# Optimization experiments

Hardware: AMD Instinct MI355X
Metric: run time of the kernel (lower is better)

## Reference

```python
import jax, jax.numpy as jnp
import numpy as np

CS = 5           # context_size
PAD = CS // 2    # spatial padding
EPS = 1e-12      # torch F.normalize eps


def setup_inputs() -> dict:
    key = jax.random.key(0)
    k1, k2, k3 = jax.random.split(key, 3)
    B, C, H, W = 8, 1024, 64, 64
    OC, INC = 1024, C + CS * CS  # 1049 input channels to 1x1 conv
    feature = jax.random.normal(k1, (B, C, H, W), dtype=jnp.float32)
    conv_w = jax.random.normal(k2, (OC, INC), dtype=jnp.float32) * 0.02
    conv_b = jax.random.normal(k3, (OC,), dtype=jnp.float32) * 0.02
    return {"feature": feature, "conv_w": conv_w, "conv_b": conv_b}


def reference(feature, conv_w, conv_b):
    b, c, h, w = feature.shape
    # L2-normalize over channel dim (torch normalize: x / max(||x||, eps))
    norm = jnp.sqrt(jnp.sum(feature * feature, axis=1, keepdims=True))
    fn = feature / jnp.maximum(norm, EPS)
    fp = jnp.pad(fn, ((0, 0), (0, 0), (PAD, PAD), (PAD, PAD)))
    # Windowed cosine-similarity cost volume: 25 fixed shifts (small static loop)
    sims = []
    for cc in range(CS):      # column shift (outer, matches torch ordering)
        for r in range(CS):   # row shift
            sims.append(jnp.sum(fp[:, :, r:h + r, cc:w + cc] * fn, axis=1))
    vol = jnp.stack(sims, axis=1)              # [b, 25, h, w]
    x = jnp.concatenate([feature, vol], axis=1)  # [b, c+25, h, w]
    # 1x1 conv == per-pixel GEMM over channels
    out = jnp.einsum('bihw,oi->bohw', x, conv_w) + conv_b[None, :, None, None]
    return jax.nn.relu(out)
```

## Files before the change

### kernel.cpp

```cpp
#include <hip/hip_runtime.h>
#include <stdint.h>

#define C_DIM 1024
#define HW    4096
#define KPAD  1056
#define KIN   1049
#define NPIX  32768

typedef __bf16 bf16x8 __attribute__((ext_vector_type(8)));
typedef float  f32x4  __attribute__((ext_vector_type(4)));
typedef unsigned short u16x8 __attribute__((ext_vector_type(8)));

typedef const __attribute__((address_space(1))) void* gas_t;
typedef __attribute__((address_space(3))) void* las_t;

__device__ __forceinline__ unsigned short f2bf(float f) {
  unsigned u = __float_as_uint(f);
  unsigned r = u + 0x7FFFu + ((u >> 16) & 1u);
  return (unsigned short)(r >> 16);
}

__global__ __launch_bounds__(256) void prep_w(const float* __restrict__ cw,
                                              unsigned short* __restrict__ wb) {
  int o = blockIdx.x;
  for (int k = threadIdx.x; k < KPAD; k += 256) {
    float v = (k < KIN) ? cw[(size_t)o * KIN + k] : 0.0f;
    wb[(size_t)o * KPAD + k] = f2bf(v);
  }
}

__global__ __launch_bounds__(256) void pack_norm(const float* __restrict__ feat,
                                                 unsigned short* __restrict__ xb,
                                                 float* __restrict__ inv_norm,
                                                 int p_base) {
  __shared__ float tile[64][65];
  __shared__ float red[4][64];
  int t   = threadIdx.x;
  int p0l = blockIdx.x * 64;
  int p0g = p_base + p0l;
  int b   = p0g >> 12;
  int hw0 = p0g & 4095;
  int pl = t & 63;
  int q  = t >> 6;
  const float* fb = feat + (size_t)b * C_DIM * HW + hw0;
  float sumsq = 0.0f;
  for (int cc = 0; cc < 16; ++cc) {
#pragma unroll
    for (int i = 0; i < 16; ++i) {
      int cl = q + 4 * i;
      float v = fb[(size_t)(cc * 64 + cl) * HW + pl];
      sumsq += v * v;
      tile[cl][pl] = v;
    }
    __syncthreads();
#pragma unroll
    for (int r = 0; r < 2; ++r) {
      int id = t + r * 256;
      int pr = id >> 3;
      int c8 = id & 7;
      u16x8 hv;
#pragma unroll
      for (int e = 0; e < 8; ++e) hv[e] = f2bf(tile[c8 * 8 + e][pr]);
      size_t row = (size_t)(p0l + pr) * KPAD + cc * 64 + c8 * 8;
      *reinterpret_cast<u16x8*>(xb + row) = hv;
    }
    __syncthreads();
  }
  red[q][pl] = sumsq;
  __syncthreads();
  if (t < 64) {
    float s = red[0][t] + red[1][t] + red[2][t] + red[3][t];
    inv_norm[p0g + t] = 1.0f / fmaxf(sqrtf(s), 1e-12f);
  }
}

__global__ __launch_bounds__(256) void corr_part(const float* __restrict__ feat,
                                                 float* __restrict__ part,
                                                 int b_base, int npix_s) {
  __shared__ float tile[4][8][72];
  int t = threadIdx.x;
  int bid = blockIdx.x;
  int chunk = bid & 3;
  int ht = (bid >> 2) & 15;
  int bl = bid >> 6;
  int b  = b_base + bl;
  int h0 = ht * 4;
  int r0 = t >> 6;
  int w  = t & 63;
  {
    int ch = t >> 6, r = (t >> 3) & 7, c = t & 7;
    int col = (c < 2) ? c : (64 + c);
    tile[ch][r][col] = 0.0f;
  }
  __syncthreads();
  const float* fb = feat + (size_t)b * C_DIM * HW;
  int c0 = chunk * 256;
  int h_lo = h0 - 2 + r0;
  int h_hi = h0 + 2 + r0;
  bool v_lo = (h_lo >= 0);
  bool v_hi = (h_hi < 64);
  size_t off_lo = (size_t)(v_lo ? h_lo : 0) * 64 + w;
  size_t off_hi = (size_t)(v_hi ? h_hi : 0) * 64 + w;
  float acc[25];
#pragma unroll
  for (int j = 0; j < 25; ++j) acc[j] = 0.0f;
  for (int ci0 = 0; ci0 < 256; ci0 += 4) {
    float lo[4], hi[4];
#pragma unroll
    for (int cc = 0; cc < 4; ++cc) {
      size_t cb = (size_t)(c0 + ci0 + cc) * HW;
      lo[cc] = v_lo ? fb[cb + off_lo] : 0.0f;
      hi[cc] = v_hi ? fb[cb + off_hi] : 0.0f;
    }
    __syncthreads();
#pragma unroll
    for (int cc = 0; cc < 4; ++cc) {
      tile[cc][r0][2 + w]     = lo[cc];
      tile[cc][r0 + 4][2 + w] = hi[cc];
    }
    __syncthreads();
#pragma unroll
    for (int cc = 0; cc < 4; ++cc) {
      float rv[5][5];
#pragma unroll
      for (int dr5 = 0; dr5 < 5; ++dr5) {
        const float* rp = &tile[cc][r0 + dr5][w];
#pragma unroll
        for (int dc5 = 0; dc5 < 5; ++dc5) rv[dr5][dc5] = rp[dc5];
      }
      float center = rv[2][2];
#pragma unroll
      for (int dc5 = 0; dc5 < 5; ++dc5)
#pragma unroll
        for (int dr5 = 0; dr5 < 5; ++dr5)
          acc[dc5 * 5 + dr5] += rv[dr5][dc5] * center;
    }
  }
  int pl = bl * 4096 + (h0 + r0) * 64 + w;
#pragma unroll
  for (int j = 0; j < 25; ++j)
    part[(size_t)(chunk * 25 + j) * npix_s + pl] = acc[j];
}

__global__ __launch_bounds__(256) void corr_reduce(const float* __restrict__ part,
                                                   const float* __restrict__ inv_norm,
                                                   unsigned short* __restrict__ xb,
                                                   int p_base, int npix_s) {
  int pl = blockIdx.x * 256 + threadIdx.x;
  int pg = p_base + pl;
  int w = pg & 63, h = (pg >> 6) & 63, b = pg >> 12;
  float inv_c = inv_norm[pg];
  float vals[32];
#pragma unroll
  for (int j = 0; j < 32; ++j) {
    float v = 0.0f;
    if (j < 25) {
      int dc = j / 5 - 2, dr = j % 5 - 2;
      int hh = h + dr, ww = w + dc;
      if (hh >= 0 && hh < 64 && ww >= 0 && ww < 64) {
        float s = part[(size_t)(0 * 25 + j) * npix_s + pl]
                + part[(size_t)(1 * 25 + j) * npix_s + pl]
                + part[(size_t)(2 * 25 + j) * npix_s + pl]
                + part[(size_t)(3 * 25 + j) * npix_s + pl];
        v = s * inv_c * inv_norm[(b << 12) + (hh << 6) + ww];
      }
    }
    vals[j] = v;
  }
  unsigned short* xp = xb + (size_t)pl * KPAD + 1024;
#pragma unroll
  for (int g = 0; g < 4; ++g) {
    u16x8 pk;
#pragma unroll
    for (int e = 0; e < 8; ++e) pk[e] = f2bf(vals[g * 8 + e]);
    *reinterpret_cast<u16x8*>(xp + g * 8) = pk;
  }
}

__device__ __forceinline__ void stage_tile(const unsigned short* __restrict__ g,
                                           unsigned short* s, int t) {
#pragma unroll
  for (int r = 0; r < 2; ++r) {
    int idx = t + r * 256;
    int row = idx >> 2;
    int q = (idx & 3) ^ ((row >> 1) & 3);
    const unsigned short* gp = g + (size_t)row * KPAD + q * 8;
    unsigned short* sp = s + (t >> 6) * 512 + r * 2048;
    __builtin_amdgcn_global_load_lds((gas_t)gp, (las_t)sp, 16, 0, 0);
  }
}

__global__ __launch_bounds__(256, 2) void gemm_kernel(
    const unsigned short* __restrict__ xb, const unsigned short* __restrict__ wb,
    const float* __restrict__ bias, float* __restrict__ out,
    int p_base, int np) {
  __shared__ __align__(16) unsigned short sA[4096];
  __shared__ __align__(16) unsigned short sB[4096];
  int t = threadIdx.x;
  int lane = t & 63;
  int wid = t >> 6;
  int wm = wid >> 1, wn = wid & 1;
  int l15 = lane & 15, l4 = lane >> 4;
  int bid = blockIdx.x;
  int xcd = bid & 7;
  int j = bid >> 3;
  int o0 = (j & 7) * 128;
  int panel = xcd * (np >> 3) + (j >> 3);
  int p0l = panel * 128;

  f32x4 acc[4][4];
#pragma unroll
  for (int m = 0; m < 4; ++m)
#pragma unroll
    for (int n = 0; n < 4; ++n)
#pragma unroll
      for (int i = 0; i < 4; ++i) acc[m][n][i] = 0.0f;

  const unsigned short* A = wb + (size_t)o0 * KPAD;
  const unsigned short* B = xb + (size_t)p0l * KPAD;

  for (int kt = 0; kt < KPAD / 32; ++kt) {
    int k0 = kt * 32;
    stage_tile(A + k0, sA, t);
    stage_tile(B + k0, sB, t);
    __syncthreads();

    bf16x8 bf[4];
#pragma unroll
    for (int n = 0; n < 4; ++n) {
      int rr = wn * 64 + n * 16 + l15;
      int off = rr * 32 + ((l4 ^ ((rr >> 1) & 3)) * 8);
      bf[n] = *reinterpret_cast<const bf16x8*>(&sB[off]);
    }
#pragma unroll
    for (int m = 0; m < 4; ++m) {
      int ra = wm * 64 + m * 16 + l15;
      int off = ra * 32 + ((l4 ^ ((ra >> 1) & 3)) * 8);
      bf16x8 af = *reinterpret_cast<const bf16x8*>(&sA[off]);
#pragma unroll
      for (int n = 0; n < 4; ++n)
        acc[m][n] = __builtin_amdgcn_mfma_f32_16x16x32_bf16(af, bf[n], acc[m][n], 0, 0, 0);
    }
    __syncthreads();
  }

#pragma unroll
  for (int m = 0; m < 4; ++m) {
    int ob = o0 + wm * 64 + m * 16 + l4 * 4;
    float b0 = bias[ob], b1 = bias[ob + 1], b2 = bias[ob + 2], b3 = bias[ob + 3];
#pragma unroll
    for (int n = 0; n < 4; ++n) {
      int pg = p_base + p0l + wn * 64 + n * 16 + l15;
      int bb = pg >> 12, hw = pg & 4095;
      float* op = out + ((size_t)bb << 22) + hw;
      op[(size_t)(ob + 0) << 12] = fmaxf(acc[m][n][0] + b0, 0.0f);
      op[(size_t)(ob + 1) << 12] = fmaxf(acc[m][n][1] + b1, 0.0f);
      op[(size_t)(ob + 2) << 12] = fmaxf(acc[m][n][2] + b2, 0.0f);
      op[(size_t)(ob + 3) << 12] = fmaxf(acc[m][n][3] + b3, 0.0f);
    }
  }
}

extern "C" void kernel_launch(void* const* d_in, const int* in_sizes, int n_in,
                              void* d_out, int out_size, void* d_ws, size_t ws_size,
                              hipStream_t stream) {
  const float* feat = (const float*)d_in[0];
  const float* cw   = (const float*)d_in[1];
  const float* cb   = (const float*)d_in[2];
  float* out = (float*)d_out;

  const int NB = 8;
  const int npix_s = NB * 4096;

  char* ws = (char*)d_ws;
  size_t SZ_XS = (size_t)npix_s * KPAD * 2;
  size_t SZ_W  = (size_t)1024 * KPAD * 2;
  unsigned short* xb = (unsigned short*)(ws);
  unsigned short* wb = (unsigned short*)(ws + SZ_XS);
  float* inv_norm    = (float*)(ws + SZ_XS + SZ_W);
  float* part        = (float*)(ws + SZ_XS + SZ_W + (size_t)NPIX * 4);

  prep_w<<<1024, 256, 0, stream>>>(cw, wb);
  pack_norm<<<NB * 64, 256, 0, stream>>>(feat, xb, inv_norm, 0);
  corr_part<<<NB * 64, 256, 0, stream>>>(feat, part, 0, npix_s);
  corr_reduce<<<npix_s / 256, 256, 0, stream>>>(part, inv_norm, xb, 0, npix_s);
  gemm_kernel<<<8 * NB * 32, 256, 0, stream>>>(xb, wb, cb, out, 0, NB * 32);
}
```

Baseline: 451.8 us.

## Retile correlation kernel into 16-row strips with 4-pixel register blocking

The correlation partial kernel is restructured. Each block now covers a 16-row strip for one of 16 channel chunks instead of 4 rows for one of 4 chunks. Each thread computes 4 adjacent pixels from vectorized LDS window reads, and tiles are filled with direct global-to-LDS loads. The aim is to cut redundant halo loads and LDS reads per output and to drop the per-iteration register staging. The cost is a partial-sum buffer four times larger, which the reduce kernel must now write and sum over 16 chunks instead of 4.

```diff
diff --git a/kernel.cpp b/kernel.cpp
--- a/kernel.cpp
+++ b/kernel.cpp
@@ -6,9 +6,11 @@
 #define KPAD  1056
 #define KIN   1049
 #define NPIX  32768
+#define NCHUNK 16
 
 typedef __bf16 bf16x8 __attribute__((ext_vector_type(8)));
 typedef float  f32x4  __attribute__((ext_vector_type(4)));
+typedef float  f32x2  __attribute__((ext_vector_type(2)));
 typedef unsigned short u16x8 __attribute__((ext_vector_type(8)));
 
 typedef const __attribute__((address_space(1))) void* gas_t;
@@ -75,81 +77,77 @@
 }
 
 __global__ __launch_bounds__(256) void corr_part(const float* __restrict__ feat,
-                                                 float* __restrict__ part,
-                                                 int b_base, int npix_s) {
-  __shared__ float tile[4][8][72];
+                                                 float* __restrict__ part) {
+  __shared__ float lds4[4 + 1280 + 4];
+  float* tile = lds4 + 4;
   int t = threadIdx.x;
   int bid = blockIdx.x;
-  int chunk = bid & 3;
-  int ht = (bid >> 2) & 15;
-  int bl = bid >> 6;
-  int b  = b_base + bl;
-  int h0 = ht * 4;
-  int r0 = t >> 6;
-  int w  = t & 63;
-  {
-    int ch = t >> 6, r = (t >> 3) & 7, c = t & 7;
-    int col = (c < 2) ? c : (64 + c);
-    tile[ch][r][col] = 0.0f;
-  }
-  __syncthreads();
+  int chunk = bid & 15;
+  int strip = (bid >> 4) & 3;
+  int b     = bid >> 6;
+  int h0 = strip * 16;
+  int hr = t >> 4;
+  int w0 = (t & 15) * 4;
+  int wid = t >> 6;
+  int lane = t & 63;
+
   const float* fb = feat + (size_t)b * C_DIM * HW;
-  int c0 = chunk * 256;
-  int h_lo = h0 - 2 + r0;
-  int h_hi = h0 + 2 + r0;
-  bool v_lo = (h_lo >= 0);
-  bool v_hi = (h_hi < 64);
-  size_t off_lo = (size_t)(v_lo ? h_lo : 0) * 64 + w;
-  size_t off_hi = (size_t)(v_hi ? h_hi : 0) * 64 + w;
-  float acc[25];
-#pragma unroll
-  for (int j = 0; j < 25; ++j) acc[j] = 0.0f;
-  for (int ci0 = 0; ci0 < 256; ci0 += 4) {
-    float lo[4], hi[4];
-#pragma unroll
-    for (int cc = 0; cc < 4; ++cc) {
-      size_t cb = (size_t)(c0 + ci0 + cc) * HW;
-      lo[cc] = v_lo ? fb[cb + off_lo] : 0.0f;
-      hi[cc] = v_hi ? fb[cb + off_hi] : 0.0f;
-    }
-    __syncthreads();
-#pragma unroll
-    for (int cc = 0; cc < 4; ++cc) {
-      tile[cc][r0][2 + w]     = lo[cc];
-      tile[cc][r0 + 4][2 + w] = hi[cc];
-    }
-    __syncthreads();
-#pragma unroll
-    for (int cc = 0; cc < 4; ++cc) {
-      float rv[5][5];
-#pragma unroll
-      for (int dr5 = 0; dr5 < 5; ++dr5) {
-        const float* rp = &tile[cc][r0 + dr5][w];
-#pragma unroll
-        for (int dc5 = 0; dc5 < 5; ++dc5) rv[dr5][dc5] = rp[dc5];
-      }
-      float center = rv[2][2];
-#pragma unroll
-      for (int dc5 = 0; dc5 < 5; ++dc5)
-#pragma unroll
-        for (int dr5 = 0; dr5 < 5; ++dr5)
-          acc[dc5 * 5 + dr5] += rv[dr5][dc5] * center;
-    }
-  }
-  int pl = bl * 4096 + (h0 + r0) * 64 + w;
-#pragma unroll
-  for (int j = 0; j < 25; ++j)
-    part[(size_t)(chunk * 25 + j) * npix_s + pl] = acc[j];
+  int rA = t >> 4;
+  int cA = (t & 15) * 4;
+  int hA = min(max(h0 - 2 + rA, 0), 63);
+  int rB = 16 + wid;
+  int cB = lane;
+  int hB = min(max(h0 - 2 + rB, 0), 63);
+  const float* srcA = fb + hA * 64 + cA;
+  const float* srcB = fb + hB * 64 + cB;
+  float* dstA = tile + wid * 256;
+  float* dstB = tile + 1024 + wid * 64;
+
+  float acc[4][25];
+#pragma unroll
+  for (int j = 0; j < 4; ++j)
+#pragma unroll
+    for (int k = 0; k < 25; ++k) acc[j][k] = 0.0f;
+
+  int c0 = chunk * 64;
+  for (int ci = 0; ci < 64; ++ci) {
+    size_t coff = (size_t)(c0 + ci) * HW;
+    __builtin_amdgcn_global_load_lds((gas_t)(srcA + coff), (las_t)dstA, 16, 0, 0);
+    __builtin_amdgcn_global_load_lds((gas_t)(srcB + coff), (las_t)dstB, 4, 0, 0);
+    __syncthreads();
+
+    const float* rp2 = tile + (hr + 2) * 64 + w0;
+    f32x4 ctr4 = *reinterpret_cast<const f32x4*>(rp2);
+#pragma unroll
+    for (int r5 = 0; r5 < 5; ++r5) {
+      const float* rp = tile + (hr + r5) * 64 + w0;
+      f32x2 eL = *reinterpret_cast<const f32x2*>(rp - 2);
+      f32x4 cc4 = *reinterpret_cast<const f32x4*>(rp);
+      f32x2 eR = *reinterpret_cast<const f32x2*>(rp + 4);
+      float win[8] = {eL[0], eL[1], cc4[0], cc4[1], cc4[2], cc4[3], eR[0], eR[1]};
+#pragma unroll
+      for (int j = 0; j < 4; ++j)
+#pragma unroll
+        for (int dcv = 0; dcv < 5; ++dcv)
+          acc[j][dcv * 5 + r5] += win[j + dcv] * ctr4[j];
+    }
+    __syncthreads();
+  }
+
+  int p0 = b * 4096 + (h0 + hr) * 64 + w0;
+#pragma unroll
+  for (int jj = 0; jj < 25; ++jj) {
+    f32x4 v = {acc[0][jj], acc[1][jj], acc[2][jj], acc[3][jj]};
+    *reinterpret_cast<f32x4*>(&part[(size_t)(chunk * 25 + jj) * NPIX + p0]) = v;
+  }
 }
 
 __global__ __launch_bounds__(256) void corr_reduce(const float* __restrict__ part,
                                                    const float* __restrict__ inv_norm,
-                                                   unsigned short* __restrict__ xb,
-                                                   int p_base, int npix_s) {
+                                                   unsigned short* __restrict__ xb) {
   int pl = blockIdx.x * 256 + threadIdx.x;
-  int pg = p_base + pl;
-  int w = pg & 63, h = (pg >> 6) & 63, b = pg >> 12;
-  float inv_c = inv_norm[pg];
+  int w = pl & 63, h = (pl >> 6) & 63, b = pl >> 12;
+  float inv_c = inv_norm[pl];
   float vals[32];
 #pragma unroll
   for (int j = 0; j < 32; ++j) {
@@ -158,10 +156,10 @@
       int dc = j / 5 - 2, dr = j % 5 - 2;
       int hh = h + dr, ww = w + dc;
       if (hh >= 0 && hh < 64 && ww >= 0 && ww < 64) {
-        float s = part[(size_t)(0 * 25 + j) * npix_s + pl]
-                + part[(size_t)(1 * 25 + j) * npix_s + pl]
-                + part[(size_t)(2 * 25 + j) * npix_s + pl]
-                + part[(size_t)(3 * 25 + j) * npix_s + pl];
+        float s = 0.0f;
+#pragma unroll
+        for (int c = 0; c < NCHUNK; ++c)
+          s += part[(size_t)(c * 25 + j) * NPIX + pl];
         v = s * inv_c * inv_norm[(b << 12) + (hh << 6) + ww];
       }
     }
@@ -269,20 +267,17 @@
   const float* cb   = (const float*)d_in[2];
   float* out = (float*)d_out;
 
-  const int NB = 8;
-  const int npix_s = NB * 4096;
-
   char* ws = (char*)d_ws;
-  size_t SZ_XS = (size_t)npix_s * KPAD * 2;
-  size_t SZ_W  = (size_t)1024 * KPAD * 2;
+  size_t SZ_X = (size_t)NPIX * KPAD * 2;
+  size_t SZ_W = (size_t)1024 * KPAD * 2;
   unsigned short* xb = (unsigned short*)(ws);
-  unsigned short* wb = (unsigned short*)(ws + SZ_XS);
-  float* inv_norm    = (float*)(ws + SZ_XS + SZ_W);
-  float* part        = (float*)(ws + SZ_XS + SZ_W + (size_t)NPIX * 4);
+  unsigned short* wb = (unsigned short*)(ws + SZ_X);
+  float* inv_norm    = (float*)(ws + SZ_X + SZ_W);
+  float* part        = (float*)(ws + SZ_X + SZ_W + (size_t)NPIX * 4);
 
   prep_w<<<1024, 256, 0, stream>>>(cw, wb);
-  pack_norm<<<NB * 64, 256, 0, stream>>>(feat, xb, inv_norm, 0);
-  corr_part<<<NB * 64, 256, 0, stream>>>(feat, part, 0, npix_s);
-  corr_reduce<<<npix_s / 256, 256, 0, stream>>>(part, inv_norm, xb, 0, npix_s);
-  gemm_kernel<<<8 * NB * 32, 256, 0, stream>>>(xb, wb, cb, out, 0, NB * 32);
-}
+  pack_norm<<<512, 256, 0, stream>>>(feat, xb, inv_norm, 0);
+  corr_part<<<512, 256, 0, stream>>>(feat, part);
+  corr_reduce<<<128, 256, 0, stream>>>(part, inv_norm, xb);
+  gemm_kernel<<<2048, 256, 0, stream>>>(xb, wb, cb, out, 0, 256);
+}
```

Result: faster. 429.5 us (-4.9%).
